# Optimization experiments

Hardware: AMD Instinct MI355X
Metric: run time of the kernel (lower is better)

Reference implementation:

```python
import jax, jax.numpy as jnp
import numpy as np

GRID_SIZE = 5
GRID_RANGE = (-1.0, 1.0)


def setup_inputs() -> dict:
    key = jax.random.key(0)
    k1, k2, k3 = jax.random.split(key, 3)
    B, D, U, K = 16384, 1024, 128, GRID_SIZE + 3  # spline_order=3
    x = jax.random.normal(k1, (B, D), dtype=jnp.float32)
    # glorot-ish scale for weights
    base_weight = jax.random.normal(k2, (D, U), dtype=jnp.float32) * (1.0 / np.sqrt(D))
    spline_weight = jax.random.normal(k3, (D, U, K), dtype=jnp.float32) * (1.0 / np.sqrt(D))
    return {"x": x, "base_weight": base_weight, "spline_weight": spline_weight}


def reference(x, base_weight, spline_weight):
    # base path: SiLU(x @ W_b)
    base_out = jax.nn.silu(x @ base_weight)  # [B, U]
    # spline path: RBF over grid centers, then contract (note: x_norm in the
    # original call() is computed but unused, so it is omitted here)
    centers = jnp.linspace(GRID_RANGE[0], GRID_RANGE[1], GRID_SIZE)  # [G]
    dist = jnp.square(x[..., None] - centers)        # [B, D, G]
    rbf = jnp.exp(-5.0 * dist)                        # [B, D, G]
    spline_out = jnp.einsum('big,iug->bu', rbf, spline_weight[:, :, :GRID_SIZE])
    return base_out + spline_out
```

## Files before the change

### kernel.cpp

```cpp
#include <hip/hip_runtime.h>

typedef unsigned short u16;
typedef unsigned int u32;
typedef __bf16 bf16x8 __attribute__((ext_vector_type(8)));
typedef float f32x16 __attribute__((ext_vector_type(16)));

#define C2 (-7.213475204444817f)
#define T1C 0.28650480f
#define T2C 0.0067379470f

__device__ __forceinline__ u16 f2bf(float f) {
  u32 u = __float_as_uint(f);
  return (u16)((u + 0x7FFFu + ((u >> 16) & 1u)) >> 16);
}

__device__ __forceinline__ f32x16 mfma16(uint4 a, uint4 b, f32x16 c) {
  return __builtin_amdgcn_mfma_f32_32x32x16_bf16(
      __builtin_bit_cast(bf16x8, a), __builtin_bit_cast(bf16x8, b), c, 0, 0, 0);
}

__global__ __launch_bounds__(256) void kan_prep(const float* __restrict__ wb,
                                                const float* __restrict__ ws,
                                                u16* __restrict__ wst3) {
  __shared__ u16 tile[6][16][130];
  const int t = threadIdx.x;
  const int c = blockIdx.x;
#pragma unroll
  for (int it = 0; it < 8; ++it) {
    int idx = it * 256 + t;
    int d = idx >> 7, u = idx & 127;
    size_t base = (size_t)(c * 16 + d) * 128 + u;
    const float* p = ws + base * 8;
    float4 v0 = *(const float4*)p;
    float g4 = p[4];
    tile[0][d][u] = f2bf(v0.x);
    tile[1][d][u] = f2bf(v0.y);
    tile[2][d][u] = f2bf(v0.z);
    tile[3][d][u] = f2bf(v0.w);
    tile[4][d][u] = f2bf(g4);
    tile[5][d][u] = f2bf(wb[base]);
  }
  __syncthreads();
#pragma unroll
  for (int i = 0; i < 6; ++i) {
    int g = i * 256 + t;
    int s = g >> 8, r = g & 255;
    int nq = r >> 6, l = r & 63;
    int u = nq * 32 + (l & 31);
    int dbase = (l >> 5) * 8;
    u32 q[4];
#pragma unroll
    for (int j = 0; j < 4; ++j) {
      u32 lo = tile[s][dbase + 2 * j][u];
      u32 hi = tile[s][dbase + 2 * j + 1][u];
      q[j] = lo | (hi << 16);
    }
    uint4 w4; w4.x = q[0]; w4.y = q[1]; w4.z = q[2]; w4.w = q[3];
    *(uint4*)(wst3 + (size_t)c * 12288 + (size_t)g * 8) = w4;
  }
}

__global__ __launch_bounds__(512, 2) void kan_main(const float* __restrict__ x,
                                                   const u16* __restrict__ wst3,
                                                   float* __restrict__ out) {
  __shared__ __align__(16) char lds[98304];

  const int t = threadIdx.x;
  const int lane = t & 63;
  const int w = t >> 6;
  const int kq = w & 3;
  const int wn = w >> 2;
  const int b0 = blockIdx.x * 64;

  f32x16 acc[8];
#pragma unroll
  for (int i = 0; i < 8; ++i)
#pragma unroll
    for (int j = 0; j < 16; ++j) acc[i][j] = 0.f;

  const int r = t >> 3, o = t & 7;
  const float* xp = x + (size_t)(b0 + r) * 1024 + o * 8;
  const u32 aw = (u32)((((r >> 5) * 4 + (o >> 1)) << 10) + ((o & 1) << 9) +
                       (((r & 31) ^ o) << 4));

  const char* bsrc = (const char*)wst3 + kq * 24576 + wn * 2048 + lane * 16;

  const u32 ar = (u32)((kq << 10) + ((lane >> 5) << 9) +
                       ((((lane & 31) ^ (kq * 2 + (lane >> 5)))) << 4));

  auto rbf_write = [&](char* buf, float4 xa, float4 xb) {
    float xf[8] = {xa.x, xa.y, xa.z, xa.w, xb.x, xb.y, xb.z, xb.w};
    u32 pk[6][4];
#pragma unroll
    for (int pp = 0; pp < 4; ++pp) {
      u32 lo6[6], hi6[6];
#pragma unroll
      for (int e = 0; e < 2; ++e) {
        float xv = xf[2 * pp + e];
        float t0 = C2 * xv;
        float P = __builtin_amdgcn_exp2f(t0 * xv);
        float Qp = __builtin_amdgcn_exp2f(-t0);
        float Qm = __builtin_amdgcn_exp2f(t0);
        float PQ = P * Qp, PQm = P * Qm;
        u32* dst = e ? hi6 : lo6;
        dst[0] = __float_as_uint(PQm * Qm * T2C) + 0x8000u;
        dst[1] = __float_as_uint(PQm * T1C) + 0x8000u;
        dst[2] = __float_as_uint(P) + 0x8000u;
        dst[3] = __float_as_uint(PQ * T1C) + 0x8000u;
        dst[4] = __float_as_uint(PQ * Qp * T2C) + 0x8000u;
        dst[5] = __float_as_uint(xv) + 0x8000u;
      }
#pragma unroll
      for (int s = 0; s < 6; ++s)
        pk[s][pp] = __builtin_amdgcn_perm(hi6[s], lo6[s], 0x07060302);
    }
#pragma unroll
    for (int s = 0; s < 6; ++s) {
      uint4 v; v.x = pk[s][0]; v.y = pk[s][1]; v.z = pk[s][2]; v.w = pk[s][3];
      *(uint4*)(buf + s * 8192 + aw) = v;
    }
  };

  float4 xc0 = *(const float4*)(xp);
  float4 xc1 = *(const float4*)(xp + 4);
  rbf_write(lds, xc0, xc1);
  xc0 = *(const float4*)(xp + 64);
  xc1 = *(const float4*)(xp + 68);
  __syncthreads();

  for (int i = 0; i < 16; ++i) {
    char* cur = lds + (size_t)(i & 1) * 49152;
    char* nxt = lds + (size_t)((i + 1) & 1) * 49152;
    const char* bc = bsrc + (size_t)i * 98304;

    uint4 av[6], bv[6];
#pragma unroll
    for (int s = 0; s < 3; ++s) {
      bv[2 * s] = *(const uint4*)(bc + s * 4096);
      bv[2 * s + 1] = *(const uint4*)(bc + s * 4096 + 1024);
      av[2 * s] = *(const uint4*)(cur + s * 8192 + ar);
      av[2 * s + 1] = *(const uint4*)(cur + s * 8192 + 4096 + ar);
    }
    if (i < 15) {
      rbf_write(nxt, xc0, xc1);
      if (i < 14) {
        xc0 = *(const float4*)(xp + (i + 2) * 64);
        xc1 = *(const float4*)(xp + (i + 2) * 64 + 4);
      }
    }
#pragma unroll
    for (int s = 0; s < 3; ++s) {
      acc[0] = mfma16(av[2 * s], bv[2 * s], acc[0]);
      acc[1] = mfma16(av[2 * s], bv[2 * s + 1], acc[1]);
      acc[2] = mfma16(av[2 * s + 1], bv[2 * s], acc[2]);
      acc[3] = mfma16(av[2 * s + 1], bv[2 * s + 1], acc[3]);
    }
#pragma unroll
    for (int s = 3; s < 6; ++s) {
      int j = 2 * (s - 3);
      bv[j] = *(const uint4*)(bc + s * 4096);
      bv[j + 1] = *(const uint4*)(bc + s * 4096 + 1024);
      av[j] = *(const uint4*)(cur + s * 8192 + ar);
      av[j + 1] = *(const uint4*)(cur + s * 8192 + 4096 + ar);
    }
#pragma unroll
    for (int s = 3; s < 5; ++s) {
      int j = 2 * (s - 3);
      acc[0] = mfma16(av[j], bv[j], acc[0]);
      acc[1] = mfma16(av[j], bv[j + 1], acc[1]);
      acc[2] = mfma16(av[j + 1], bv[j], acc[2]);
      acc[3] = mfma16(av[j + 1], bv[j + 1], acc[3]);
    }
    acc[4] = mfma16(av[4], bv[4], acc[4]);
    acc[5] = mfma16(av[4], bv[5], acc[5]);
    acc[6] = mfma16(av[5], bv[4], acc[6]);
    acc[7] = mfma16(av[5], bv[5], acc[7]);
    __syncthreads();
  }

#pragma unroll
  for (int q = 0; q < 4; ++q) {
    if (kq != 0) {
      char* slab = lds + ((kq - 1) * 2 + wn) * 8192;
#pragma unroll
      for (int rq = 0; rq < 4; ++rq) {
        *(float4*)(slab + rq * 1024 + lane * 16) =
            make_float4(acc[q][4 * rq], acc[q][4 * rq + 1],
                        acc[q][4 * rq + 2], acc[q][4 * rq + 3]);
        *(float4*)(slab + 4096 + rq * 1024 + lane * 16) =
            make_float4(acc[4 + q][4 * rq], acc[4 + q][4 * rq + 1],
                        acc[4 + q][4 * rq + 2], acc[4 + q][4 * rq + 3]);
      }
    }
    __syncthreads();
    if (kq == 0) {
#pragma unroll
      for (int p = 1; p < 4; ++p) {
        const char* slab = lds + ((p - 1) * 2 + wn) * 8192;
#pragma unroll
        for (int rq = 0; rq < 4; ++rq) {
          float4 vs = *(const float4*)(slab + rq * 1024 + lane * 16);
          float4 vb = *(const float4*)(slab + 4096 + rq * 1024 + lane * 16);
          acc[q][4 * rq] += vs.x; acc[q][4 * rq + 1] += vs.y;
          acc[q][4 * rq + 2] += vs.z; acc[q][4 * rq + 3] += vs.w;
          acc[4 + q][4 * rq] += vb.x; acc[4 + q][4 * rq + 1] += vb.y;
          acc[4 + q][4 * rq + 2] += vb.z; acc[4 + q][4 * rq + 3] += vb.w;
        }
      }
      const int col = wn * 64 + (q & 1) * 32 + (lane & 31);
#pragma unroll
      for (int reg = 0; reg < 16; ++reg) {
        int row = (q >> 1) * 32 + (reg & 3) + 8 * (reg >> 2) + 4 * (lane >> 5);
        float z = acc[4 + q][reg];
        float sv = z / (1.0f + __expf(-z));
        out[(size_t)(b0 + row) * 128 + col] = sv + acc[q][reg];
      }
    }
    __syncthreads();
  }
}

extern "C" void kernel_launch(void* const* d_in, const int* in_sizes, int n_in,
                              void* d_out, int out_size, void* d_ws, size_t ws_size,
                              hipStream_t stream) {
  const float* x  = (const float*)d_in[0];
  const float* wb = (const float*)d_in[1];
  const float* ws = (const float*)d_in[2];
  u16* wst3 = (u16*)d_ws;
  float* out = (float*)d_out;

  kan_prep<<<dim3(64), 256, 0, stream>>>(wb, ws, wst3);
  kan_main<<<dim3(256), 512, 0, stream>>>(x, wst3, out);
}
```

Baseline: 137.3 us.

## Shrink batch tile to 32 rows with 4 K-split waves per block

Moves kan_main from 64-row tiles with 8 waves (2 N-halves × 4 K-quarters) to 32-row tiles with 4 waves, each covering all 128 output columns for its K-quarter. Blocks double to 512 and LDS per block halves, which aims at more resident blocks and better spread across CUs. B-fragments are loaded in two batches of registers, and the MFMA section is wrapped in s_setprio. The cost is that each wave reloads the full weight slice for only 32 rows, doubling global weight traffic per output row, and B-fragment register pressure rises.

```diff
diff --git a/kernel.cpp b/kernel.cpp
--- a/kernel.cpp
+++ b/kernel.cpp
@@ -60,33 +60,32 @@
   }
 }
 
-__global__ __launch_bounds__(512, 2) void kan_main(const float* __restrict__ x,
+__global__ __launch_bounds__(256, 2) void kan_main(const float* __restrict__ x,
                                                    const u16* __restrict__ wst3,
                                                    float* __restrict__ out) {
-  __shared__ __align__(16) char lds[98304];
+  __shared__ __align__(16) char lds[49152];
 
   const int t = threadIdx.x;
   const int lane = t & 63;
-  const int w = t >> 6;
-  const int kq = w & 3;
-  const int wn = w >> 2;
-  const int b0 = blockIdx.x * 64;
-
-  f32x16 acc[8];
-#pragma unroll
-  for (int i = 0; i < 8; ++i)
-#pragma unroll
-    for (int j = 0; j < 16; ++j) acc[i][j] = 0.f;
+  const int kq = t >> 6;
+  const int b0 = blockIdx.x * 32;
 
   const int r = t >> 3, o = t & 7;
+  const u32 aw = ((u32)(o >> 1) << 10) + ((u32)(o & 1) << 9) +
+                 ((u32)((r ^ o) & 31) << 4);
   const float* xp = x + (size_t)(b0 + r) * 1024 + o * 8;
-  const u32 aw = (u32)((((r >> 5) * 4 + (o >> 1)) << 10) + ((o & 1) << 9) +
-                       (((r & 31) ^ o) << 4));
-
-  const char* bsrc = (const char*)wst3 + kq * 24576 + wn * 2048 + lane * 16;
-
-  const u32 ar = (u32)((kq << 10) + ((lane >> 5) << 9) +
-                       ((((lane & 31) ^ (kq * 2 + (lane >> 5)))) << 4));
+
+  const int m = lane & 31, kh = lane >> 5;
+  const u32 ar = ((u32)kq << 10) + ((u32)kh << 9) +
+                 ((u32)((m ^ (kq * 2 + kh)) & 31) << 4);
+
+  const char* bsrc = (const char*)wst3 + (size_t)kq * 24576 + lane * 16;
+
+  f32x16 sp[4], ba[4];
+#pragma unroll
+  for (int i = 0; i < 4; ++i)
+#pragma unroll
+    for (int j = 0; j < 16; ++j) { sp[i][j] = 0.f; ba[i][j] = 0.f; }
 
   auto rbf_write = [&](char* buf, float4 xa, float4 xb) {
     float xf[8] = {xa.x, xa.y, xa.z, xa.w, xb.x, xb.y, xb.z, xb.w};
@@ -117,7 +116,7 @@
 #pragma unroll
     for (int s = 0; s < 6; ++s) {
       uint4 v; v.x = pk[s][0]; v.y = pk[s][1]; v.z = pk[s][2]; v.w = pk[s][3];
-      *(uint4*)(buf + s * 8192 + aw) = v;
+      *(uint4*)(buf + s * 4096 + aw) = v;
     }
   };
 
@@ -129,18 +128,17 @@
   __syncthreads();
 
   for (int i = 0; i < 16; ++i) {
-    char* cur = lds + (size_t)(i & 1) * 49152;
-    char* nxt = lds + (size_t)((i + 1) & 1) * 49152;
+    char* cur = lds + (i & 1) * 24576;
+    char* nxt = lds + ((i + 1) & 1) * 24576;
     const char* bc = bsrc + (size_t)i * 98304;
 
-    uint4 av[6], bv[6];
-#pragma unroll
-    for (int s = 0; s < 3; ++s) {
-      bv[2 * s] = *(const uint4*)(bc + s * 4096);
-      bv[2 * s + 1] = *(const uint4*)(bc + s * 4096 + 1024);
-      av[2 * s] = *(const uint4*)(cur + s * 8192 + ar);
-      av[2 * s + 1] = *(const uint4*)(cur + s * 8192 + 4096 + ar);
-    }
+    uint4 bvA[3][4];
+#pragma unroll
+    for (int s = 0; s < 3; ++s)
+#pragma unroll
+      for (int nt = 0; nt < 4; ++nt)
+        bvA[s][nt] = *(const uint4*)(bc + s * 4096 + nt * 1024);
+
     if (i < 15) {
       rbf_write(nxt, xc0, xc1);
       if (i < 14) {
@@ -148,72 +146,88 @@
         xc1 = *(const float4*)(xp + (i + 2) * 64 + 4);
       }
     }
+
+    uint4 bvB[3][4];
+#pragma unroll
+    for (int s = 0; s < 3; ++s)
+#pragma unroll
+      for (int nt = 0; nt < 4; ++nt)
+        bvB[s][nt] = *(const uint4*)(bc + (s + 3) * 4096 + nt * 1024);
+
+    __builtin_amdgcn_s_setprio(1);
 #pragma unroll
     for (int s = 0; s < 3; ++s) {
-      acc[0] = mfma16(av[2 * s], bv[2 * s], acc[0]);
-      acc[1] = mfma16(av[2 * s], bv[2 * s + 1], acc[1]);
-      acc[2] = mfma16(av[2 * s + 1], bv[2 * s], acc[2]);
-      acc[3] = mfma16(av[2 * s + 1], bv[2 * s + 1], acc[3]);
-    }
-#pragma unroll
-    for (int s = 3; s < 6; ++s) {
-      int j = 2 * (s - 3);
-      bv[j] = *(const uint4*)(bc + s * 4096);
-      bv[j + 1] = *(const uint4*)(bc + s * 4096 + 1024);
-      av[j] = *(const uint4*)(cur + s * 8192 + ar);
-      av[j + 1] = *(const uint4*)(cur + s * 8192 + 4096 + ar);
-    }
-#pragma unroll
-    for (int s = 3; s < 5; ++s) {
-      int j = 2 * (s - 3);
-      acc[0] = mfma16(av[j], bv[j], acc[0]);
-      acc[1] = mfma16(av[j], bv[j + 1], acc[1]);
-      acc[2] = mfma16(av[j + 1], bv[j], acc[2]);
-      acc[3] = mfma16(av[j + 1], bv[j + 1], acc[3]);
-    }
-    acc[4] = mfma16(av[4], bv[4], acc[4]);
-    acc[5] = mfma16(av[4], bv[5], acc[5]);
-    acc[6] = mfma16(av[5], bv[4], acc[6]);
-    acc[7] = mfma16(av[5], bv[5], acc[7]);
+      uint4 av = *(const uint4*)(cur + s * 4096 + ar);
+#pragma unroll
+      for (int nt = 0; nt < 4; ++nt) sp[nt] = mfma16(av, bvA[s][nt], sp[nt]);
+    }
+#pragma unroll
+    for (int s = 0; s < 2; ++s) {
+      uint4 av = *(const uint4*)(cur + (s + 3) * 4096 + ar);
+#pragma unroll
+      for (int nt = 0; nt < 4; ++nt) sp[nt] = mfma16(av, bvB[s][nt], sp[nt]);
+    }
+    {
+      uint4 av = *(const uint4*)(cur + 5 * 4096 + ar);
+#pragma unroll
+      for (int nt = 0; nt < 4; ++nt) ba[nt] = mfma16(av, bvB[2][nt], ba[nt]);
+    }
+    __builtin_amdgcn_s_setprio(0);
     __syncthreads();
   }
 
 #pragma unroll
-  for (int q = 0; q < 4; ++q) {
+  for (int rd = 0; rd < 2; ++rd) {
     if (kq != 0) {
-      char* slab = lds + ((kq - 1) * 2 + wn) * 8192;
+      char* slab = lds + (kq - 1) * 16384;
 #pragma unroll
       for (int rq = 0; rq < 4; ++rq) {
-        *(float4*)(slab + rq * 1024 + lane * 16) =
-            make_float4(acc[q][4 * rq], acc[q][4 * rq + 1],
-                        acc[q][4 * rq + 2], acc[q][4 * rq + 3]);
-        *(float4*)(slab + 4096 + rq * 1024 + lane * 16) =
-            make_float4(acc[4 + q][4 * rq], acc[4 + q][4 * rq + 1],
-                        acc[4 + q][4 * rq + 2], acc[4 + q][4 * rq + 3]);
+        *(float4*)(slab + 0 * 4096 + rq * 1024 + lane * 16) =
+            make_float4(sp[2 * rd][4 * rq], sp[2 * rd][4 * rq + 1],
+                        sp[2 * rd][4 * rq + 2], sp[2 * rd][4 * rq + 3]);
+        *(float4*)(slab + 1 * 4096 + rq * 1024 + lane * 16) =
+            make_float4(sp[2 * rd + 1][4 * rq], sp[2 * rd + 1][4 * rq + 1],
+                        sp[2 * rd + 1][4 * rq + 2], sp[2 * rd + 1][4 * rq + 3]);
+        *(float4*)(slab + 2 * 4096 + rq * 1024 + lane * 16) =
+            make_float4(ba[2 * rd][4 * rq], ba[2 * rd][4 * rq + 1],
+                        ba[2 * rd][4 * rq + 2], ba[2 * rd][4 * rq + 3]);
+        *(float4*)(slab + 3 * 4096 + rq * 1024 + lane * 16) =
+            make_float4(ba[2 * rd + 1][4 * rq], ba[2 * rd + 1][4 * rq + 1],
+                        ba[2 * rd + 1][4 * rq + 2], ba[2 * rd + 1][4 * rq + 3]);
       }
     }
     __syncthreads();
     if (kq == 0) {
 #pragma unroll
       for (int p = 1; p < 4; ++p) {
-        const char* slab = lds + ((p - 1) * 2 + wn) * 8192;
+        const char* slab = lds + (p - 1) * 16384;
 #pragma unroll
         for (int rq = 0; rq < 4; ++rq) {
-          float4 vs = *(const float4*)(slab + rq * 1024 + lane * 16);
-          float4 vb = *(const float4*)(slab + 4096 + rq * 1024 + lane * 16);
-          acc[q][4 * rq] += vs.x; acc[q][4 * rq + 1] += vs.y;
-          acc[q][4 * rq + 2] += vs.z; acc[q][4 * rq + 3] += vs.w;
-          acc[4 + q][4 * rq] += vb.x; acc[4 + q][4 * rq + 1] += vb.y;
-          acc[4 + q][4 * rq + 2] += vb.z; acc[4 + q][4 * rq + 3] += vb.w;
+          float4 v0 = *(const float4*)(slab + 0 * 4096 + rq * 1024 + lane * 16);
+          float4 v1 = *(const float4*)(slab + 1 * 4096 + rq * 1024 + lane * 16);
+          float4 v2 = *(const float4*)(slab + 2 * 4096 + rq * 1024 + lane * 16);
+          float4 v3 = *(const float4*)(slab + 3 * 4096 + rq * 1024 + lane * 16);
+          sp[2 * rd][4 * rq] += v0.x; sp[2 * rd][4 * rq + 1] += v0.y;
+          sp[2 * rd][4 * rq + 2] += v0.z; sp[2 * rd][4 * rq + 3] += v0.w;
+          sp[2 * rd + 1][4 * rq] += v1.x; sp[2 * rd + 1][4 * rq + 1] += v1.y;
+          sp[2 * rd + 1][4 * rq + 2] += v1.z; sp[2 * rd + 1][4 * rq + 3] += v1.w;
+          ba[2 * rd][4 * rq] += v2.x; ba[2 * rd][4 * rq + 1] += v2.y;
+          ba[2 * rd][4 * rq + 2] += v2.z; ba[2 * rd][4 * rq + 3] += v2.w;
+          ba[2 * rd + 1][4 * rq] += v3.x; ba[2 * rd + 1][4 * rq + 1] += v3.y;
+          ba[2 * rd + 1][4 * rq + 2] += v3.z; ba[2 * rd + 1][4 * rq + 3] += v3.w;
         }
       }
-      const int col = wn * 64 + (q & 1) * 32 + (lane & 31);
-#pragma unroll
-      for (int reg = 0; reg < 16; ++reg) {
-        int row = (q >> 1) * 32 + (reg & 3) + 8 * (reg >> 2) + 4 * (lane >> 5);
-        float z = acc[4 + q][reg];
-        float sv = z / (1.0f + __expf(-z));
-        out[(size_t)(b0 + row) * 128 + col] = sv + acc[q][reg];
+#pragma unroll
+      for (int nti = 0; nti < 2; ++nti) {
+        const int nt = 2 * rd + nti;
+        const int col = nt * 32 + (lane & 31);
+#pragma unroll
+        for (int reg = 0; reg < 16; ++reg) {
+          int row = (reg & 3) + 8 * (reg >> 2) + 4 * (lane >> 5);
+          float z = ba[nt][reg];
+          float sv = z / (1.0f + __expf(-z));
+          out[(size_t)(b0 + row) * 128 + col] = sv + sp[nt][reg];
+        }
       }
     }
     __syncthreads();
@@ -230,5 +244,5 @@
   float* out = (float*)d_out;
 
   kan_prep<<<dim3(64), 256, 0, stream>>>(wb, ws, wst3);
-  kan_main<<<dim3(256), 512, 0, stream>>>(x, wst3, out);
-}
+  kan_main<<<dim3(512), 256, 0, stream>>>(x, wst3, out);
+}
```

After: 138.3 us. About the same (+0.8%).
